# Performance work log

Hardware: AMD Instinct MI355X
Metric: run time of the kernel (lower is better)

The kernel has to match this reference:

```python
import jax, jax.numpy as jnp
import numpy as np

B, L, D_MODEL = 2, 2048, 1024
D_INNER, D_STATE, D_CONV, DT_RANK = 2048, 16, 4, 64  # expand=2, dt_rank=ceil(1024/16)


def setup_inputs() -> dict:
    key = jax.random.key(0)
    ks = jax.random.split(key, 12)
    s = lambda k, shape, sc=0.02: jax.random.normal(k, shape, dtype=jnp.float32) * sc
    return {
        "x": jax.random.normal(ks[0], (B, L, D_MODEL), dtype=jnp.float32),
        "norm_w": jnp.ones((D_MODEL,), jnp.float32),
        "norm_b": jnp.zeros((D_MODEL,), jnp.float32),
        "in_proj_w": s(ks[1], (2 * D_INNER, D_MODEL)),
        "conv_w": s(ks[2], (D_INNER, 1, D_CONV), 0.1),
        "conv_b": s(ks[3], (D_INNER,), 0.1),
        "x_proj_w": s(ks[4], (DT_RANK + 2 * D_STATE, D_INNER)),
        "dt_proj_w": s(ks[5], (D_INNER, DT_RANK), 0.1),
        "dt_proj_b": s(ks[6], (D_INNER,), 0.5),
        "A_log": jnp.log(jnp.broadcast_to(jnp.arange(1, D_STATE + 1, dtype=jnp.float32), (D_INNER, D_STATE))),
        "D": jnp.ones((D_INNER,), jnp.float32),
        "out_proj_w": s(ks[7], (D_MODEL, D_INNER)),
    }


def _layernorm(x, w, b, eps=1e-5):
    mu = jnp.mean(x, axis=-1, keepdims=True)
    var = jnp.var(x, axis=-1, keepdims=True)
    return (x - mu) * jax.lax.rsqrt(var + eps) * w + b


def _mamba_forward(x, norm_w, norm_b, in_proj_w, conv_w, conv_b, x_proj_w,
                   dt_proj_w, dt_proj_b, A_log, D, out_proj_w):
    residual = x
    xn = _layernorm(x, norm_w, norm_b)
    # in_proj -> split into x-branch and gate z
    xz = jnp.einsum('bld,ed->ble', xn, in_proj_w)  # [B,L,2*D_INNER]
    xc, z = jnp.split(xz, 2, axis=-1)
    # causal depthwise conv1d over time
    xt = jnp.transpose(xc, (0, 2, 1))  # [B,C,L]
    xt = jnp.pad(xt, ((0, 0), (0, 0), (D_CONV - 1, 0)))
    xt = jax.lax.conv_general_dilated(
        xt, conv_w, window_strides=(1,), padding=[(0, 0)],
        feature_group_count=D_INNER,
        dimension_numbers=('NCH', 'OIH', 'NCH')) + conv_b[None, :, None]
    u = jax.nn.silu(jnp.transpose(xt, (0, 2, 1)))  # [B,L,D_INNER]
    # input-dependent dt, B, C
    x_dbl = jnp.einsum('bld,ed->ble', u, x_proj_w)
    dt, Bm, Cm = jnp.split(x_dbl, [DT_RANK, DT_RANK + D_STATE], axis=-1)
    dt = jax.nn.softplus(jnp.einsum('blr,dr->bld', dt, dt_proj_w) + dt_proj_b)  # [B,L,D_INNER]
    A = -jnp.exp(A_log)  # [D_INNER, D_STATE]

    def step(h, inp):
        dt_t, B_t, C_t, u_t = inp  # [B,Di],[B,Ds],[B,Ds],[B,Di]
        dA = jnp.exp(dt_t[..., None] * A)                       # [B,Di,Ds]
        h = dA * h + (dt_t * u_t)[..., None] * B_t[:, None, :]  # [B,Di,Ds]
        y_t = jnp.einsum('bds,bs->bd', h, C_t)
        return h, y_t

    xs = (jnp.transpose(dt, (1, 0, 2)), jnp.transpose(Bm, (1, 0, 2)),
          jnp.transpose(Cm, (1, 0, 2)), jnp.transpose(u, (1, 0, 2)))
    h0 = jnp.zeros((B, D_INNER, D_STATE), dtype=x.dtype)
    _, ys = jax.lax.scan(step, h0, xs)
    y = jnp.transpose(ys, (1, 0, 2)) + u * D  # [B,L,D_INNER]
    y = y * jax.nn.silu(z)
    out = jnp.einsum('ble,de->bld', y, out_proj_w)
    # dropout in eval mode = identity
    return residual + out


def reference(x, norm_w, norm_b, in_proj_w, conv_w, conv_b, x_proj_w,
              dt_proj_w, dt_proj_b, A_log, D, out_proj_w):
    return _mamba_forward(x, norm_w, norm_b, in_proj_w, conv_w, conv_b, x_proj_w,
                          dt_proj_w, dt_proj_b, A_log, D, out_proj_w)
```

## Files before the change

### kernel.cpp

```cpp
#include <hip/hip_runtime.h>
#include <hip/hip_bf16.h>
#include <math.h>

#define BB 2
#define LL 2048
#define DMODEL 1024
#define DINNER 2048
#define DSTATE 16
#define DTRANK 64
#define NROWS (BB * LL)
#define NC 32
#define CK 64

typedef __bf16 bf16x8 __attribute__((ext_vector_type(8)));
typedef float  f32x4  __attribute__((ext_vector_type(4)));
typedef __attribute__((address_space(3))) void       as3_void;
typedef const __attribute__((address_space(1))) void as1_cvoid;

__device__ __forceinline__ ushort f2bf(float x) {
    __hip_bfloat16 h = __float2bfloat16(x);
    return *(ushort*)&h;
}

__global__ __launch_bounds__(256) void ln_kernel(const float* __restrict__ x,
                                                 const float* __restrict__ w,
                                                 const float* __restrict__ b,
                                                 __hip_bfloat16* __restrict__ xn) {
    int row = blockIdx.x;
    const float* xr = x + (size_t)row * DMODEL;
    float4 v = reinterpret_cast<const float4*>(xr)[threadIdx.x];
    float s  = v.x + v.y + v.z + v.w;
    float ss = v.x * v.x + v.y * v.y + v.z * v.z + v.w * v.w;
    for (int off = 32; off > 0; off >>= 1) {
        s  += __shfl_down(s, off);
        ss += __shfl_down(ss, off);
    }
    __shared__ float red0[4], red1[4];
    __shared__ float mu_s, rstd_s;
    int lane = threadIdx.x & 63, wv = threadIdx.x >> 6;
    if (lane == 0) { red0[wv] = s; red1[wv] = ss; }
    __syncthreads();
    if (threadIdx.x == 0) {
        float S = red0[0] + red0[1] + red0[2] + red0[3];
        float SS = red1[0] + red1[1] + red1[2] + red1[3];
        float mu = S * (1.0f / DMODEL);
        float var = SS * (1.0f / DMODEL) - mu * mu;
        mu_s = mu;
        rstd_s = rsqrtf(var + 1e-5f);
    }
    __syncthreads();
    float mu = mu_s, rstd = rstd_s;
    float4 wv4 = reinterpret_cast<const float4*>(w)[threadIdx.x];
    float4 bv4 = reinterpret_cast<const float4*>(b)[threadIdx.x];
    ushort4 o;
    o.x = f2bf((v.x - mu) * rstd * wv4.x + bv4.x);
    o.y = f2bf((v.y - mu) * rstd * wv4.y + bv4.y);
    o.z = f2bf((v.z - mu) * rstd * wv4.z + bv4.z);
    o.w = f2bf((v.w - mu) * rstd * wv4.w + bv4.w);
    *reinterpret_cast<ushort4*>((ushort*)xn + (size_t)row * DMODEL + threadIdx.x * 4) = o;
}

__global__ __launch_bounds__(256) void cvt_kernel(const float* __restrict__ in,
                                                  __hip_bfloat16* __restrict__ o) {
    int i = (blockIdx.x * 256 + threadIdx.x) * 4;
    float4 v = *reinterpret_cast<const float4*>(in + i);
    ushort4 p;
    p.x = f2bf(v.x); p.y = f2bf(v.y); p.z = f2bf(v.z); p.w = f2bf(v.w);
    *reinterpret_cast<ushort4*>((ushort*)o + i) = p;
}

template <int EPI>
__global__ __launch_bounds__(256) void gemm_bf16(
    const __hip_bfloat16* __restrict__ A, int lda,
    const __hip_bfloat16* __restrict__ W, int ldw,
    float* __restrict__ C, float* __restrict__ C2, int nsplit, int ldc,
    int K, const float* __restrict__ R) {
    __shared__ ushort As[128][32];
    __shared__ ushort Bs[128][32];
    int tid = threadIdx.x;
    int w = tid >> 6, lane = tid & 63;
    int m0 = blockIdx.y * 128, n0 = blockIdx.x * 128;
    int wr = w >> 1, wc = w & 1;

    int srow = (w << 4) + (lane >> 2);
    int skoff = (lane & 3) << 3;
    const ushort* gA = (const ushort*)A + (size_t)(m0 + srow) * lda + skoff;
    const ushort* gB = (const ushort*)W + (size_t)(n0 + srow) * ldw + skoff;
    char* ldsA0 = (char*)&As[0][0] + w * 1024;
    char* ldsB0 = (char*)&Bs[0][0] + w * 1024;

    f32x4 acc[4][4] = {};
    int frow = (lane & 15);
    int fk   = (lane >> 4) << 3;

    for (int k0 = 0; k0 < K; k0 += 32) {
        __syncthreads();
        __builtin_amdgcn_global_load_lds((as1_cvoid*)(gA + k0),                 (as3_void*)(ldsA0),        16, 0, 0);
        __builtin_amdgcn_global_load_lds((as1_cvoid*)(gA + (size_t)64 * lda + k0), (as3_void*)(ldsA0 + 4096), 16, 0, 0);
        __builtin_amdgcn_global_load_lds((as1_cvoid*)(gB + k0),                 (as3_void*)(ldsB0),        16, 0, 0);
        __builtin_amdgcn_global_load_lds((as1_cvoid*)(gB + (size_t)64 * ldw + k0), (as3_void*)(ldsB0 + 4096), 16, 0, 0);
        __syncthreads();

        bf16x8 af[4], bfr[4];
#pragma unroll
        for (int mi = 0; mi < 4; mi++)
            af[mi] = *(const bf16x8*)&As[wr * 64 + mi * 16 + frow][fk];
#pragma unroll
        for (int ni = 0; ni < 4; ni++)
            bfr[ni] = *(const bf16x8*)&Bs[wc * 64 + ni * 16 + frow][fk];
#pragma unroll
        for (int mi = 0; mi < 4; mi++)
#pragma unroll
            for (int ni = 0; ni < 4; ni++)
                acc[mi][ni] = __builtin_amdgcn_mfma_f32_16x16x32_bf16(
                    af[mi], bfr[ni], acc[mi][ni], 0, 0, 0);
    }

    int crow = (lane >> 4) << 2;
    int ccol = lane & 15;
    float* Cb = C;
    int nbase = n0;
    if (EPI == 0 && n0 >= nsplit) { Cb = C2; nbase = n0 - nsplit; }
#pragma unroll
    for (int mi = 0; mi < 4; mi++) {
#pragma unroll
        for (int ni = 0; ni < 4; ni++) {
#pragma unroll
            for (int r = 0; r < 4; r++) {
                int m = m0 + wr * 64 + mi * 16 + crow + r;
                int n = nbase + wc * 64 + ni * 16 + ccol;
                float v = acc[mi][ni][r];
                if (EPI == 2) v += R[(size_t)m * ldc + n];
                Cb[(size_t)m * ldc + n] = v;
            }
        }
    }
}

template <int EPI>
__global__ __launch_bounds__(256) void gemm_kernel(
    const float* __restrict__ A, int lda,
    const float* __restrict__ W, int ldw,
    float* __restrict__ C, int ldc,
    int N, int K,
    const float* __restrict__ bias) {
    __shared__ float As[16][64];
    __shared__ float Ws[16][64];
    int m0 = blockIdx.y * 64;
    int n0 = blockIdx.x * 64;
    int tid = threadIdx.x;
    int tm = tid >> 4, tn = tid & 15;
    int lr = tid >> 2;
    int lk = (tid & 3) << 2;

    float acc[4][4] = {};

    for (int k0 = 0; k0 < K; k0 += 16) {
        float4 av = *reinterpret_cast<const float4*>(A + (size_t)(m0 + lr) * lda + k0 + lk);
        float4 wvv;
        int wn = n0 + lr;
        if (wn < N)
            wvv = *reinterpret_cast<const float4*>(W + (size_t)wn * ldw + k0 + lk);
        else
            wvv = make_float4(0.f, 0.f, 0.f, 0.f);
        __syncthreads();
        As[lk + 0][lr] = av.x; As[lk + 1][lr] = av.y;
        As[lk + 2][lr] = av.z; As[lk + 3][lr] = av.w;
        Ws[lk + 0][lr] = wvv.x; Ws[lk + 1][lr] = wvv.y;
        Ws[lk + 2][lr] = wvv.z; Ws[lk + 3][lr] = wvv.w;
        __syncthreads();
#pragma unroll
        for (int k = 0; k < 16; k++) {
            float4 a = *reinterpret_cast<const float4*>(&As[k][tm << 2]);
            float4 bv = *reinterpret_cast<const float4*>(&Ws[k][tn << 2]);
            float ar[4] = {a.x, a.y, a.z, a.w};
            float br[4] = {bv.x, bv.y, bv.z, bv.w};
#pragma unroll
            for (int i = 0; i < 4; i++)
#pragma unroll
                for (int j = 0; j < 4; j++)
                    acc[i][j] = fmaf(ar[i], br[j], acc[i][j]);
        }
    }
#pragma unroll
    for (int i = 0; i < 4; i++) {
        int m = m0 + (tm << 2) + i;
#pragma unroll
        for (int j = 0; j < 4; j++) {
            int n = n0 + (tn << 2) + j;
            if (n < N) {
                float v = acc[i][j];
                if (EPI == 1) {
                    v += bias[n];
                    v = (v > 20.f) ? v : log1pf(__expf(v));
                }
                C[(size_t)m * ldc + n] = v;
            }
        }
    }
}

__global__ __launch_bounds__(256) void conv_silu_kernel(
    const float* __restrict__ xc, const float* __restrict__ cw,
    const float* __restrict__ cb, float* __restrict__ u) {
    int c = blockIdx.x * 256 + threadIdx.x;
    int r = blockIdx.y;
    int l = r & (LL - 1);
    float4 wv = reinterpret_cast<const float4*>(cw)[c];
    const float* p = xc + (size_t)r * DINNER + c;
    float acc = cb[c];
    if (l >= 3) acc = fmaf(p[-3 * DINNER], wv.x, acc);
    if (l >= 2) acc = fmaf(p[-2 * DINNER], wv.y, acc);
    if (l >= 1) acc = fmaf(p[-1 * DINNER], wv.z, acc);
    acc = fmaf(p[0], wv.w, acc);
    float sig = 1.f / (1.f + __expf(-acc));
    u[(size_t)r * DINNER + c] = acc * sig;
}

__global__ __launch_bounds__(256) void scan_pass1(
    const float* __restrict__ dt, const float* __restrict__ u,
    const float* __restrict__ xdbl, const float* __restrict__ A_log,
    float* __restrict__ hloc, float* __restrict__ aprod) {
    int bc = blockIdx.x >> 3;
    int b = bc >> 5, c = bc & (NC - 1);
    int d = ((blockIdx.x & 7) << 8) + threadIdx.x;
    float a2[DSTATE];
#pragma unroll
    for (int s = 0; s < DSTATE; s++)
        a2[s] = -__expf(A_log[d * DSTATE + s]) * 1.44269504089f;
    float h[DSTATE], ap[DSTATE];
#pragma unroll
    for (int s = 0; s < DSTATE; s++) { h[s] = 0.f; ap[s] = 1.f; }

    int t0 = c * CK;
    const float* dtp = dt + ((size_t)b * LL + t0) * DINNER + d;
    const float* up  = u  + ((size_t)b * LL + t0) * DINNER + d;
    const float* xr0 = xdbl + ((size_t)b * LL + t0) * 96;

    for (int t = 0; t < CK; t++) {
        float dtv = dtp[(size_t)t * DINNER];
        float uv  = up[(size_t)t * DINNER];
        float du  = dtv * uv;
        const float* xr = xr0 + t * 96;
#pragma unroll
        for (int s = 0; s < DSTATE; s++) {
            float dA = exp2f(dtv * a2[s]);
            h[s] = fmaf(dA, h[s], du * xr[64 + s]);
            ap[s] *= dA;
        }
    }
    size_t base = ((size_t)bc * DSTATE) * DINNER + d;
#pragma unroll
    for (int s = 0; s < DSTATE; s++) {
        hloc[base + (size_t)s * DINNER]  = h[s];
        aprod[base + (size_t)s * DINNER] = ap[s];
    }
}

__global__ __launch_bounds__(256) void scan_pass2(
    float* __restrict__ hloc, const float* __restrict__ aprod) {
    int idx = blockIdx.x * 256 + threadIdx.x;
    int d = idx & (DINNER - 1);
    int s = (idx >> 11) & (DSTATE - 1);
    int b = idx >> 15;
    float run = 0.f;
    for (int c = 0; c < NC; c++) {
        size_t off = ((size_t)((b * NC + c) * DSTATE + s)) * DINNER + d;
        float hl = hloc[off];
        float ap = aprod[off];
        hloc[off] = run;
        run = fmaf(ap, run, hl);
    }
}

__global__ __launch_bounds__(256) void scan_pass3(
    const float* __restrict__ dt, const float* __restrict__ u,
    const float* __restrict__ xdbl, const float* __restrict__ zb,
    const float* __restrict__ A_log, const float* __restrict__ Dp,
    const float* __restrict__ hinit, __hip_bfloat16* __restrict__ y) {
    int bc = blockIdx.x >> 3;
    int b = bc >> 5, c = bc & (NC - 1);
    int d = ((blockIdx.x & 7) << 8) + threadIdx.x;
    float a2[DSTATE];
#pragma unroll
    for (int s = 0; s < DSTATE; s++)
        a2[s] = -__expf(A_log[d * DSTATE + s]) * 1.44269504089f;
    float Dd = Dp[d];
    float h[DSTATE];
    size_t base = ((size_t)bc * DSTATE) * DINNER + d;
#pragma unroll
    for (int s = 0; s < DSTATE; s++) h[s] = hinit[base + (size_t)s * DINNER];

    int t0 = c * CK;
    const float* dtp = dt + ((size_t)b * LL + t0) * DINNER + d;
    const float* up  = u  + ((size_t)b * LL + t0) * DINNER + d;
    const float* zp  = zb + ((size_t)b * LL + t0) * DINNER + d;
    const float* xr0 = xdbl + ((size_t)b * LL + t0) * 96;
    ushort* yp = (ushort*)y + ((size_t)b * LL + t0) * DINNER + d;

    for (int t = 0; t < CK; t++) {
        float dtv = dtp[(size_t)t * DINNER];
        float uv  = up[(size_t)t * DINNER];
        float du  = dtv * uv;
        const float* xr = xr0 + t * 96;
        float yv = 0.f;
#pragma unroll
        for (int s = 0; s < DSTATE; s++) {
            float dA = exp2f(dtv * a2[s]);
            h[s] = fmaf(dA, h[s], du * xr[64 + s]);
            yv = fmaf(h[s], xr[80 + s], yv);
        }
        float zv = zp[(size_t)t * DINNER];
        float sig = 1.f / (1.f + __expf(-zv));
        yv = (yv + uv * Dd) * (zv * sig);
        yp[(size_t)t * DINNER] = f2bf(yv);
    }
}

extern "C" void kernel_launch(void* const* d_in, const int* in_sizes, int n_in,
                              void* d_out, int out_size, void* d_ws, size_t ws_size,
                              hipStream_t stream) {
    const float* x         = (const float*)d_in[0];
    const float* norm_w    = (const float*)d_in[1];
    const float* norm_b    = (const float*)d_in[2];
    const float* in_proj_w = (const float*)d_in[3];
    const float* conv_w    = (const float*)d_in[4];
    const float* conv_b    = (const float*)d_in[5];
    const float* x_proj_w  = (const float*)d_in[6];
    const float* dt_proj_w = (const float*)d_in[7];
    const float* dt_proj_b = (const float*)d_in[8];
    const float* A_log     = (const float*)d_in[9];
    const float* Dp        = (const float*)d_in[10];
    const float* out_proj_w= (const float*)d_in[11];
    float* out = (float*)d_out;

    float* ws   = (float*)d_ws;
    const size_t NI = (size_t)NROWS * DINNER;
    float* xc   = ws;
    float* zb   = xc + NI;
    float* u    = zb + NI;
    float* dtb  = u + NI;
    float* xdbl = dtb + NI;
    __hip_bfloat16* xnb = (__hip_bfloat16*)(xdbl + (size_t)NROWS * 96);
    __hip_bfloat16* ybb = xnb + (size_t)NROWS * DMODEL;
    __hip_bfloat16* wib = ybb + NI;
    __hip_bfloat16* wob = wib + (size_t)2 * DINNER * DMODEL;
    float* hloc  = xc;
    float* aprod = xc + (size_t)BB * NC * DSTATE * DINNER;

    ln_kernel<<<NROWS, 256, 0, stream>>>(x, norm_w, norm_b, xnb);
    cvt_kernel<<<(2 * DINNER * DMODEL) / 1024, 256, 0, stream>>>(in_proj_w, wib);
    cvt_kernel<<<(DMODEL * DINNER) / 1024, 256, 0, stream>>>(out_proj_w, wob);
    gemm_bf16<0><<<dim3((2 * DINNER) / 128, NROWS / 128), 256, 0, stream>>>(
        xnb, DMODEL, wib, DMODEL, xc, zb, DINNER, DINNER, DMODEL, nullptr);
    conv_silu_kernel<<<dim3(DINNER / 256, NROWS), 256, 0, stream>>>(xc, conv_w, conv_b, u);
    gemm_kernel<0><<<dim3(2, NROWS / 64), 256, 0, stream>>>(
        u, DINNER, x_proj_w, DINNER, xdbl, 96, 96, DINNER, nullptr);
    gemm_kernel<1><<<dim3(DINNER / 64, NROWS / 64), 256, 0, stream>>>(
        xdbl, 96, dt_proj_w, DTRANK, dtb, DINNER, DINNER, DTRANK, dt_proj_b);
    scan_pass1<<<BB * NC * (DINNER / 256), 256, 0, stream>>>(dtb, u, xdbl, A_log, hloc, aprod);
    scan_pass2<<<(BB * DSTATE * DINNER) / 256, 256, 0, stream>>>(hloc, aprod);
    scan_pass3<<<BB * NC * (DINNER / 256), 256, 0, stream>>>(dtb, u, xdbl, zb, A_log, Dp, hloc, ybb);
    gemm_bf16<2><<<dim3(DMODEL / 128, NROWS / 128), 256, 0, stream>>>(
        ybb, DINNER, wob, DINNER, out, nullptr, 1 << 30, DMODEL, DINNER, x);
}
```

Baseline: 487.6 us.

## Fuse dt_proj into scan passes, split-K x_proj, store z and u in bf16

The dt_proj GEMM and softplus are dropped as a separate kernel. Each scan thread now computes dt inline from a transposed dt_proj weight row held in registers, so the full fp32 dt tensor is never written or read twice. The x_proj GEMM, which had only 128 blocks, becomes split-K with a reduction kernel to raise parallelism. z and u are kept in bf16 for the scan passes, and the chunk count is doubled with half-length chunks. In exchange each scan pass repeats the 64-wide dot product per timestep, carries 64 extra registers per thread, and loses some precision on z and u.

```diff
diff --git a/kernel.cpp b/kernel.cpp
--- a/kernel.cpp
+++ b/kernel.cpp
@@ -9,8 +9,10 @@
 #define DSTATE 16
 #define DTRANK 64
 #define NROWS (BB * LL)
-#define NC 32
-#define CK 64
+#define NC 64
+#define CK 32
+#define KS 16
+#define KCH (DINNER / KS)
 
 typedef __bf16 bf16x8 __attribute__((ext_vector_type(8)));
 typedef float  f32x4  __attribute__((ext_vector_type(4)));
@@ -20,6 +22,10 @@
 __device__ __forceinline__ ushort f2bf(float x) {
     __hip_bfloat16 h = __float2bfloat16(x);
     return *(ushort*)&h;
+}
+__device__ __forceinline__ float bf2f(ushort u) {
+    unsigned int v = ((unsigned int)u) << 16;
+    return *(float*)&v;
 }
 
 __global__ __launch_bounds__(256) void ln_kernel(const float* __restrict__ x,
@@ -69,6 +75,14 @@
     *reinterpret_cast<ushort4*>((ushort*)o + i) = p;
 }
 
+__global__ __launch_bounds__(256) void tpw_kernel(const float* __restrict__ in,
+                                                  float* __restrict__ o) {
+    int i = blockIdx.x * 256 + threadIdx.x;
+    int r = i >> 11;
+    int d = i & (DINNER - 1);
+    o[i] = in[d * DTRANK + r];
+}
+
 template <int EPI>
 __global__ __launch_bounds__(256) void gemm_bf16(
     const __hip_bfloat16* __restrict__ A, int lda,
@@ -95,9 +109,9 @@
 
     for (int k0 = 0; k0 < K; k0 += 32) {
         __syncthreads();
-        __builtin_amdgcn_global_load_lds((as1_cvoid*)(gA + k0),                 (as3_void*)(ldsA0),        16, 0, 0);
+        __builtin_amdgcn_global_load_lds((as1_cvoid*)(gA + k0),                    (as3_void*)(ldsA0),        16, 0, 0);
         __builtin_amdgcn_global_load_lds((as1_cvoid*)(gA + (size_t)64 * lda + k0), (as3_void*)(ldsA0 + 4096), 16, 0, 0);
-        __builtin_amdgcn_global_load_lds((as1_cvoid*)(gB + k0),                 (as3_void*)(ldsB0),        16, 0, 0);
+        __builtin_amdgcn_global_load_lds((as1_cvoid*)(gB + k0),                    (as3_void*)(ldsB0),        16, 0, 0);
         __builtin_amdgcn_global_load_lds((as1_cvoid*)(gB + (size_t)64 * ldw + k0), (as3_void*)(ldsB0 + 4096), 16, 0, 0);
         __syncthreads();
 
@@ -118,9 +132,8 @@
 
     int crow = (lane >> 4) << 2;
     int ccol = lane & 15;
-    float* Cb = C;
-    int nbase = n0;
-    if (EPI == 0 && n0 >= nsplit) { Cb = C2; nbase = n0 - nsplit; }
+    bool toz = (EPI == 0) && (n0 >= nsplit);
+    int nbase = toz ? (n0 - nsplit) : n0;
 #pragma unroll
     for (int mi = 0; mi < 4; mi++) {
 #pragma unroll
@@ -131,23 +144,24 @@
                 int n = nbase + wc * 64 + ni * 16 + ccol;
                 float v = acc[mi][ni][r];
                 if (EPI == 2) v += R[(size_t)m * ldc + n];
-                Cb[(size_t)m * ldc + n] = v;
+                if (toz)
+                    ((ushort*)C2)[(size_t)m * ldc + n] = f2bf(v);
+                else
+                    C[(size_t)m * ldc + n] = v;
             }
         }
     }
 }
 
-template <int EPI>
-__global__ __launch_bounds__(256) void gemm_kernel(
-    const float* __restrict__ A, int lda,
-    const float* __restrict__ W, int ldw,
-    float* __restrict__ C, int ldc,
-    int N, int K,
-    const float* __restrict__ bias) {
+__global__ __launch_bounds__(256) void xp_partial(
+    const float* __restrict__ A,
+    const float* __restrict__ W,
+    float* __restrict__ P) {
     __shared__ float As[16][64];
     __shared__ float Ws[16][64];
     int m0 = blockIdx.y * 64;
     int n0 = blockIdx.x * 64;
+    int kbase = blockIdx.z * KCH;
     int tid = threadIdx.x;
     int tm = tid >> 4, tn = tid & 15;
     int lr = tid >> 2;
@@ -155,12 +169,12 @@
 
     float acc[4][4] = {};
 
-    for (int k0 = 0; k0 < K; k0 += 16) {
-        float4 av = *reinterpret_cast<const float4*>(A + (size_t)(m0 + lr) * lda + k0 + lk);
+    for (int k0 = kbase; k0 < kbase + KCH; k0 += 16) {
+        float4 av = *reinterpret_cast<const float4*>(A + (size_t)(m0 + lr) * DINNER + k0 + lk);
         float4 wvv;
         int wn = n0 + lr;
-        if (wn < N)
-            wvv = *reinterpret_cast<const float4*>(W + (size_t)wn * ldw + k0 + lk);
+        if (wn < 96)
+            wvv = *reinterpret_cast<const float4*>(W + (size_t)wn * DINNER + k0 + lk);
         else
             wvv = make_float4(0.f, 0.f, 0.f, 0.f);
         __syncthreads();
@@ -182,27 +196,33 @@
                     acc[i][j] = fmaf(ar[i], br[j], acc[i][j]);
         }
     }
+    float* Pz = P + (size_t)blockIdx.z * NROWS * 96;
 #pragma unroll
     for (int i = 0; i < 4; i++) {
         int m = m0 + (tm << 2) + i;
 #pragma unroll
         for (int j = 0; j < 4; j++) {
             int n = n0 + (tn << 2) + j;
-            if (n < N) {
-                float v = acc[i][j];
-                if (EPI == 1) {
-                    v += bias[n];
-                    v = (v > 20.f) ? v : log1pf(__expf(v));
-                }
-                C[(size_t)m * ldc + n] = v;
-            }
+            if (n < 96)
+                Pz[(size_t)m * 96 + n] = acc[i][j];
         }
     }
+}
+
+__global__ __launch_bounds__(256) void xp_reduce(
+    const float* __restrict__ P, float* __restrict__ xdbl) {
+    int i = blockIdx.x * 256 + threadIdx.x;
+    float s = 0.f;
+#pragma unroll
+    for (int z = 0; z < KS; z++)
+        s += P[(size_t)z * NROWS * 96 + i];
+    xdbl[i] = s;
 }
 
 __global__ __launch_bounds__(256) void conv_silu_kernel(
     const float* __restrict__ xc, const float* __restrict__ cw,
-    const float* __restrict__ cb, float* __restrict__ u) {
+    const float* __restrict__ cb, float* __restrict__ u32,
+    ushort* __restrict__ u16) {
     int c = blockIdx.x * 256 + threadIdx.x;
     int r = blockIdx.y;
     int l = r & (LL - 1);
@@ -214,16 +234,37 @@
     if (l >= 1) acc = fmaf(p[-1 * DINNER], wv.z, acc);
     acc = fmaf(p[0], wv.w, acc);
     float sig = 1.f / (1.f + __expf(-acc));
-    u[(size_t)r * DINNER + c] = acc * sig;
+    float uv = acc * sig;
+    u32[(size_t)r * DINNER + c] = uv;
+    u16[(size_t)r * DINNER + c] = f2bf(uv);
+}
+
+__device__ __forceinline__ float dt_compute(const float* __restrict__ xr,
+                                            const float* wrow, float bias) {
+    float s0 = 0.f, s1 = 0.f, s2 = 0.f, s3 = 0.f;
+#pragma unroll
+    for (int r = 0; r < DTRANK; r += 4) {
+        s0 = fmaf(wrow[r + 0], xr[r + 0], s0);
+        s1 = fmaf(wrow[r + 1], xr[r + 1], s1);
+        s2 = fmaf(wrow[r + 2], xr[r + 2], s2);
+        s3 = fmaf(wrow[r + 3], xr[r + 3], s3);
+    }
+    float v = (s0 + s1) + (s2 + s3) + bias;
+    return (v > 20.f) ? v : log1pf(__expf(v));
 }
 
 __global__ __launch_bounds__(256) void scan_pass1(
-    const float* __restrict__ dt, const float* __restrict__ u,
-    const float* __restrict__ xdbl, const float* __restrict__ A_log,
+    const ushort* __restrict__ u16, const float* __restrict__ xdbl,
+    const float* __restrict__ wtT, const float* __restrict__ dt_b,
+    const float* __restrict__ A_log,
     float* __restrict__ hloc, float* __restrict__ aprod) {
     int bc = blockIdx.x >> 3;
-    int b = bc >> 5, c = bc & (NC - 1);
+    int b = bc >> 6, c = bc & (NC - 1);
     int d = ((blockIdx.x & 7) << 8) + threadIdx.x;
+    float wrow[DTRANK];
+#pragma unroll
+    for (int r = 0; r < DTRANK; r++) wrow[r] = wtT[r * DINNER + d];
+    float dbias = dt_b[d];
     float a2[DSTATE];
 #pragma unroll
     for (int s = 0; s < DSTATE; s++)
@@ -233,15 +274,14 @@
     for (int s = 0; s < DSTATE; s++) { h[s] = 0.f; ap[s] = 1.f; }
 
     int t0 = c * CK;
-    const float* dtp = dt + ((size_t)b * LL + t0) * DINNER + d;
-    const float* up  = u  + ((size_t)b * LL + t0) * DINNER + d;
+    const ushort* up = u16 + ((size_t)b * LL + t0) * DINNER + d;
     const float* xr0 = xdbl + ((size_t)b * LL + t0) * 96;
 
     for (int t = 0; t < CK; t++) {
-        float dtv = dtp[(size_t)t * DINNER];
-        float uv  = up[(size_t)t * DINNER];
+        float uv = bf2f(up[(size_t)t * DINNER]);
+        const float* xr = xr0 + t * 96;
+        float dtv = dt_compute(xr, wrow, dbias);
         float du  = dtv * uv;
-        const float* xr = xr0 + t * 96;
 #pragma unroll
         for (int s = 0; s < DSTATE; s++) {
             float dA = exp2f(dtv * a2[s]);
@@ -274,13 +314,18 @@
 }
 
 __global__ __launch_bounds__(256) void scan_pass3(
-    const float* __restrict__ dt, const float* __restrict__ u,
-    const float* __restrict__ xdbl, const float* __restrict__ zb,
+    const ushort* __restrict__ u16, const float* __restrict__ xdbl,
+    const float* __restrict__ wtT, const float* __restrict__ dt_b,
+    const ushort* __restrict__ zb,
     const float* __restrict__ A_log, const float* __restrict__ Dp,
     const float* __restrict__ hinit, __hip_bfloat16* __restrict__ y) {
     int bc = blockIdx.x >> 3;
-    int b = bc >> 5, c = bc & (NC - 1);
+    int b = bc >> 6, c = bc & (NC - 1);
     int d = ((blockIdx.x & 7) << 8) + threadIdx.x;
+    float wrow[DTRANK];
+#pragma unroll
+    for (int r = 0; r < DTRANK; r++) wrow[r] = wtT[r * DINNER + d];
+    float dbias = dt_b[d];
     float a2[DSTATE];
 #pragma unroll
     for (int s = 0; s < DSTATE; s++)
@@ -292,17 +337,16 @@
     for (int s = 0; s < DSTATE; s++) h[s] = hinit[base + (size_t)s * DINNER];
 
     int t0 = c * CK;
-    const float* dtp = dt + ((size_t)b * LL + t0) * DINNER + d;
-    const float* up  = u  + ((size_t)b * LL + t0) * DINNER + d;
-    const float* zp  = zb + ((size_t)b * LL + t0) * DINNER + d;
+    const ushort* up = u16 + ((size_t)b * LL + t0) * DINNER + d;
+    const ushort* zp = zb  + ((size_t)b * LL + t0) * DINNER + d;
     const float* xr0 = xdbl + ((size_t)b * LL + t0) * 96;
     ushort* yp = (ushort*)y + ((size_t)b * LL + t0) * DINNER + d;
 
     for (int t = 0; t < CK; t++) {
-        float dtv = dtp[(size_t)t * DINNER];
-        float uv  = up[(size_t)t * DINNER];
+        float uv = bf2f(up[(size_t)t * DINNER]);
+        const float* xr = xr0 + t * 96;
+        float dtv = dt_compute(xr, wrow, dbias);
         float du  = dtv * uv;
-        const float* xr = xr0 + t * 96;
         float yv = 0.f;
 #pragma unroll
         for (int s = 0; s < DSTATE; s++) {
@@ -310,7 +354,7 @@
             h[s] = fmaf(dA, h[s], du * xr[64 + s]);
             yv = fmaf(h[s], xr[80 + s], yv);
         }
-        float zv = zp[(size_t)t * DINNER];
+        float zv = bf2f(zp[(size_t)t * DINNER]);
         float sig = 1.f / (1.f + __expf(-zv));
         yv = (yv + uv * Dd) * (zv * sig);
         yp[(size_t)t * DINNER] = f2bf(yv);
@@ -336,31 +380,36 @@
 
     float* ws   = (float*)d_ws;
     const size_t NI = (size_t)NROWS * DINNER;
-    float* xc   = ws;
-    float* zb   = xc + NI;
-    float* u    = zb + NI;
-    float* dtb  = u + NI;
-    float* xdbl = dtb + NI;
-    __hip_bfloat16* xnb = (__hip_bfloat16*)(xdbl + (size_t)NROWS * 96);
+    float* xc    = ws;
+    float* zbF   = xc + NI;
+    ushort* zb   = (ushort*)zbF;
+    float* u32   = zbF + NI / 2;
+    ushort* u16  = (ushort*)(u32 + NI);
+    float* xdbl  = u32 + NI + NI / 2;
+    float* wtT   = xdbl + (size_t)NROWS * 96;
+    __hip_bfloat16* xnb = (__hip_bfloat16*)(wtT + (size_t)DTRANK * DINNER);
     __hip_bfloat16* ybb = xnb + (size_t)NROWS * DMODEL;
     __hip_bfloat16* wib = ybb + NI;
     __hip_bfloat16* wob = wib + (size_t)2 * DINNER * DMODEL;
     float* hloc  = xc;
     float* aprod = xc + (size_t)BB * NC * DSTATE * DINNER;
+    float* xpp   = xc;
 
     ln_kernel<<<NROWS, 256, 0, stream>>>(x, norm_w, norm_b, xnb);
     cvt_kernel<<<(2 * DINNER * DMODEL) / 1024, 256, 0, stream>>>(in_proj_w, wib);
     cvt_kernel<<<(DMODEL * DINNER) / 1024, 256, 0, stream>>>(out_proj_w, wob);
+    tpw_kernel<<<(DTRANK * DINNER) / 256, 256, 0, stream>>>(dt_proj_w, wtT);
     gemm_bf16<0><<<dim3((2 * DINNER) / 128, NROWS / 128), 256, 0, stream>>>(
-        xnb, DMODEL, wib, DMODEL, xc, zb, DINNER, DINNER, DMODEL, nullptr);
-    conv_silu_kernel<<<dim3(DINNER / 256, NROWS), 256, 0, stream>>>(xc, conv_w, conv_b, u);
-    gemm_kernel<0><<<dim3(2, NROWS / 64), 256, 0, stream>>>(
-        u, DINNER, x_proj_w, DINNER, xdbl, 96, 96, DINNER, nullptr);
-    gemm_kernel<1><<<dim3(DINNER / 64, NROWS / 64), 256, 0, stream>>>(
-        xdbl, 96, dt_proj_w, DTRANK, dtb, DINNER, DINNER, DTRANK, dt_proj_b);
-    scan_pass1<<<BB * NC * (DINNER / 256), 256, 0, stream>>>(dtb, u, xdbl, A_log, hloc, aprod);
+        xnb, DMODEL, wib, DMODEL, xc, zbF, DINNER, DINNER, DMODEL, nullptr);
+    conv_silu_kernel<<<dim3(DINNER / 256, NROWS), 256, 0, stream>>>(
+        xc, conv_w, conv_b, u32, u16);
+    xp_partial<<<dim3(2, NROWS / 64, KS), 256, 0, stream>>>(u32, x_proj_w, xpp);
+    xp_reduce<<<(NROWS * 96) / 256, 256, 0, stream>>>(xpp, xdbl);
+    scan_pass1<<<BB * NC * (DINNER / 256), 256, 0, stream>>>(
+        u16, xdbl, wtT, dt_proj_b, A_log, hloc, aprod);
     scan_pass2<<<(BB * DSTATE * DINNER) / 256, 256, 0, stream>>>(hloc, aprod);
-    scan_pass3<<<BB * NC * (DINNER / 256), 256, 0, stream>>>(dtb, u, xdbl, zb, A_log, Dp, hloc, ybb);
+    scan_pass3<<<BB * NC * (DINNER / 256), 256, 0, stream>>>(
+        u16, xdbl, wtT, dt_proj_b, zb, A_log, Dp, hloc, ybb);
     gemm_bf16<2><<<dim3(DMODEL / 128, NROWS / 128), 256, 0, stream>>>(
         ybb, DINNER, wob, DINNER, out, nullptr, 1 << 30, DMODEL, DINNER, x);
 }
```

New measurement: 529.5 us. 8.6% more time.
